# Kernel tuning notes

Measured on AMD Instinct MI355X. Metric: run time of the kernel, lower is better.

## Reference

```python
import jax, jax.numpy as jnp
import numpy as np

DIM = 768
NUM_HEADS = 12
HEAD_DIM = DIM // NUM_HEADS
HIDDEN = 4 * DIM
EPS = 1e-6


def _linear_params(key, fan_in, fan_out):
    kw, kb = jax.random.split(key)
    bound = 1.0 / np.sqrt(fan_in)
    W = jax.random.uniform(kw, (fan_in, fan_out), jnp.float32, -bound, bound)
    b = jax.random.uniform(kb, (fan_out,), jnp.float32, -bound, bound)
    return W, b


def setup_inputs() -> dict:
    key = jax.random.key(0)
    ks = jax.random.split(key, 8)
    x = jax.random.normal(ks[0], (64, 197, DIM), jnp.float32)
    Wq, bq = _linear_params(ks[1], DIM, DIM)
    Wk, bk = _linear_params(ks[2], DIM, DIM)
    Wv, bv = _linear_params(ks[3], DIM, DIM)
    Wo, bo = _linear_params(ks[4], DIM, DIM)
    W1, b1 = _linear_params(ks[5], DIM, HIDDEN)
    W2, b2 = _linear_params(ks[6], HIDDEN, DIM)
    g1 = jnp.ones((DIM,), jnp.float32); be1 = jnp.zeros((DIM,), jnp.float32)
    g2 = jnp.ones((DIM,), jnp.float32); be2 = jnp.zeros((DIM,), jnp.float32)
    return {"x": x, "Wq": Wq, "bq": bq, "Wk": Wk, "bk": bk, "Wv": Wv, "bv": bv,
            "Wo": Wo, "bo": bo, "W1": W1, "b1": b1, "W2": W2, "b2": b2,
            "g1": g1, "be1": be1, "g2": g2, "be2": be2}


def _layernorm(x, g, b):
    mu = jnp.mean(x, axis=-1, keepdims=True)
    var = jnp.mean(jnp.square(x - mu), axis=-1, keepdims=True)
    return (x - mu) * jax.lax.rsqrt(var + EPS) * g + b


def reference(x, Wq, bq, Wk, bk, Wv, bv, Wo, bo, W1, b1, W2, b2, g1, be1, g2, be2):
    B, S, D = x.shape
    # --- attention (dropout = identity at inference) ---
    q = (x @ Wq + bq).reshape(B, S, NUM_HEADS, HEAD_DIM)
    k = (x @ Wk + bk).reshape(B, S, NUM_HEADS, HEAD_DIM)
    v = (x @ Wv + bv).reshape(B, S, NUM_HEADS, HEAD_DIM)
    scale = 1.0 / np.sqrt(HEAD_DIM).astype(np.float32)
    scores = jnp.einsum('bshd,bthd->bhst', q, k) * scale  # [B,H,S,S]
    attn = jax.nn.softmax(scores, axis=-1)
    ctx = jnp.einsum('bhst,bthd->bshd', attn, v).reshape(B, S, D)
    attn_out = ctx @ Wo + bo
    x = x + _layernorm(attn_out, g1, be1)
    # --- MLP (exact GELU, dropout = identity) ---
    h = jax.nn.gelu(x @ W1 + b1, approximate=False)
    mlp_out = h @ W2 + b2
    x = x + _layernorm(mlp_out, g2, be2)
    return x
```

## Files before the change

### kernel.cpp

```cpp
#include <hip/hip_runtime.h>
#include <hip/hip_bf16.h>
#include <math.h>

#define TOK   12608
#define DMODEL 768
#define QKVN  2304
#define HID   3072
#define NH    12
#define SEQ   197
#define SPAD  256
#define SROW  208
#define NBH   768

typedef __attribute__((ext_vector_type(8))) __bf16 bf16x8;
typedef __attribute__((ext_vector_type(4))) float  f32x4;

__device__ __forceinline__ unsigned short f2b(float f){
  unsigned u = __builtin_bit_cast(unsigned, f);
  u += 0x7FFFu + ((u >> 16) & 1u);
  return (unsigned short)(u >> 16);
}
__device__ __forceinline__ float b2f(unsigned short h){
  unsigned u = ((unsigned)h) << 16;
  return __builtin_bit_cast(float, u);
}

#define GLD16(g, l) __builtin_amdgcn_global_load_lds( \
    (const __attribute__((address_space(1))) void*)(g), \
    (__attribute__((address_space(3))) void*)(l), 16, 0, 0)

__global__ void cvt_x(const float* __restrict__ x, unsigned short* __restrict__ xb, int n){
  int idx = (blockIdx.x * blockDim.x + threadIdx.x) * 4;
  if (idx < n){
    float4 v = *reinterpret_cast<const float4*>(x + idx);
    ushort4 o; o.x = f2b(v.x); o.y = f2b(v.y); o.z = f2b(v.z); o.w = f2b(v.w);
    *reinterpret_cast<ushort4*>(xb + idx) = o;
  }
}

__global__ void wt_t(const float* __restrict__ W, unsigned short* __restrict__ Wt, int K, int N){
  __shared__ float tile[32][33];
  int k0 = blockIdx.y * 32, n0 = blockIdx.x * 32;
  int tx = threadIdx.x & 31, ty = threadIdx.x >> 5;
#pragma unroll
  for (int i = 0; i < 32; i += 8)
    tile[ty + i][tx] = W[(size_t)(k0 + ty + i) * N + n0 + tx];
  __syncthreads();
#pragma unroll
  for (int i = 0; i < 32; i += 8)
    Wt[(size_t)(n0 + ty + i) * K + k0 + tx] = f2b(tile[tx][ty + i]);
}

__global__ void cat_bias(const float* __restrict__ a, const float* __restrict__ b,
                         const float* __restrict__ c, float* __restrict__ o){
  int i = blockIdx.x * blockDim.x + threadIdx.x;
  if (i < 768) o[i] = a[i];
  else if (i < 1536) o[i] = b[i - 768];
  else if (i < 2304) o[i] = c[i - 1536];
}

template<int ACT>
__global__ __launch_bounds__(256)
void gemm_nt(const unsigned short* __restrict__ A,
             const unsigned short* __restrict__ Bt,
             const float* __restrict__ bias,
             unsigned short* __restrict__ C,
             int M, int N, int K)
{
  __shared__ unsigned short As[128 * 32];
  __shared__ unsigned short Bs[128 * 32];
  const int nb = N >> 7;
  const int bm = blockIdx.x / nb;
  const int bn = blockIdx.x - bm * nb;
  const int m0 = bm << 7, n0 = bn << 7;
  const int tid = threadIdx.x;
  const int lane = tid & 63;
  const int wid = tid >> 6;

  const int r  = tid >> 2;
  const int kk = (tid & 3) << 3;
  const unsigned short* gA1 = A  + (size_t)min(m0 + r,      M - 1) * K + kk;
  const unsigned short* gA2 = A  + (size_t)min(m0 + r + 64, M - 1) * K + kk;
  const unsigned short* gB1 = Bt + (size_t)(n0 + r)      * K + kk;
  const unsigned short* gB2 = Bt + (size_t)(n0 + r + 64) * K + kk;

  char* ldsA = (char*)As + wid * 1024;
  char* ldsB = (char*)Bs + wid * 1024;

  const int fr = lane & 15;
  const int kg = (lane >> 4) << 3;
  const int wm = (wid >> 1) << 6;
  const int wn = (wid & 1) << 6;

  f32x4 acc[4][4] = {};

  for (int kt = 0; kt < K; kt += 32){
    __syncthreads();
    GLD16(gA1 + kt, ldsA);
    GLD16(gA2 + kt, ldsA + 4096);
    GLD16(gB1 + kt, ldsB);
    GLD16(gB2 + kt, ldsB + 4096);
    __syncthreads();

    bf16x8 af[4], bfv[4];
#pragma unroll
    for (int i = 0; i < 4; i++)
      af[i]  = *reinterpret_cast<const bf16x8*>(&As[(wm + i * 16 + fr) * 32 + kg]);
#pragma unroll
    for (int i = 0; i < 4; i++)
      bfv[i] = *reinterpret_cast<const bf16x8*>(&Bs[(wn + i * 16 + fr) * 32 + kg]);
#pragma unroll
    for (int mi = 0; mi < 4; mi++)
#pragma unroll
      for (int ni = 0; ni < 4; ni++)
        acc[mi][ni] = __builtin_amdgcn_mfma_f32_16x16x32_bf16(af[mi], bfv[ni], acc[mi][ni], 0, 0, 0);
  }

  const int rbase = m0 + wm + ((lane >> 4) << 2);
#pragma unroll
  for (int ni = 0; ni < 4; ni++){
    const int cc = n0 + wn + ni * 16 + fr;
    const float bv = bias[cc];
#pragma unroll
    for (int mi = 0; mi < 4; mi++){
      const int rr0 = rbase + mi * 16;
#pragma unroll
      for (int j = 0; j < 4; j++){
        int rr = rr0 + j;
        if (rr < M){
          float v = acc[mi][ni][j] + bv;
          if (ACT == 1) v = 0.5f * v * (1.0f + erff(v * 0.70710678118f));
          C[(size_t)rr * N + cc] = f2b(v);
        }
      }
    }
  }
}

__global__ __launch_bounds__(256)
void attn_scores(const unsigned short* __restrict__ qkv, unsigned short* __restrict__ P)
{
  const int gid = blockIdx.x;
  const int nt = gid & 1;
  const int mt = (gid >> 1) % 7;
  const int bh = gid / 14;
  const int b = bh / NH, h = bh - b * NH;
  const int lane = threadIdx.x & 63, wid = threadIdx.x >> 6;
  const int m0 = mt * 32 + (wid >> 1) * 16;
  const int n0 = nt * 128 + (wid & 1) * 64;
  const size_t qbase = (size_t)b * SEQ * QKVN + h * 64;
  const size_t kbase = qbase + 768;
  const int fr = lane & 15;
  const int kg = (lane >> 4) << 3;
  const int ar = min(m0 + fr, SEQ - 1);

  f32x4 acc[4] = {};
#pragma unroll
  for (int ks = 0; ks < 64; ks += 32){
    bf16x8 af = *reinterpret_cast<const bf16x8*>(&qkv[qbase + (size_t)ar * QKVN + ks + kg]);
#pragma unroll
    for (int ni = 0; ni < 4; ni++){
      int t = min(n0 + ni * 16 + fr, SEQ - 1);
      bf16x8 bv = *reinterpret_cast<const bf16x8*>(&qkv[kbase + (size_t)t * QKVN + ks + kg]);
      acc[ni] = __builtin_amdgcn_mfma_f32_16x16x32_bf16(af, bv, acc[ni], 0, 0, 0);
    }
  }
  const int rbase = m0 + ((lane >> 4) << 2);
#pragma unroll
  for (int ni = 0; ni < 4; ni++){
    int cc = n0 + ni * 16 + fr;
#pragma unroll
    for (int j = 0; j < 4; j++){
      int rr = rbase + j;
      if (rr < SEQ)
        P[((size_t)bh * SROW + rr) * SPAD + cc] = f2b(acc[ni][j] * 0.125f);
    }
  }
}

__global__ __launch_bounds__(256)
void softmax_k(unsigned short* __restrict__ P)
{
  const int idx = blockIdx.x * 4 + (threadIdx.x >> 6);
  const int bh = idx / SEQ;
  const int s  = idx - bh * SEQ;
  unsigned short* p = P + ((size_t)bh * SROW + s) * SPAD;
  const int lane = threadIdx.x & 63;
  float v[4];
  ushort4 u = *reinterpret_cast<const ushort4*>(p + lane * 4);
  v[0] = b2f(u.x); v[1] = b2f(u.y); v[2] = b2f(u.z); v[3] = b2f(u.w);
  float m = -1e30f;
#pragma unroll
  for (int j = 0; j < 4; j++){
    if (lane * 4 + j < SEQ) m = fmaxf(m, v[j]); else v[j] = -1e30f;
  }
#pragma unroll
  for (int o = 32; o > 0; o >>= 1) m = fmaxf(m, __shfl_xor(m, o));
  float sum = 0.f;
#pragma unroll
  for (int j = 0; j < 4; j++){ v[j] = __expf(v[j] - m); sum += v[j]; }
#pragma unroll
  for (int o = 32; o > 0; o >>= 1) sum += __shfl_xor(sum, o);
  const float inv = 1.0f / sum;
  ushort4 o4;
  o4.x = f2b(v[0] * inv); o4.y = f2b(v[1] * inv);
  o4.z = f2b(v[2] * inv); o4.w = f2b(v[3] * inv);
  *reinterpret_cast<ushort4*>(p + lane * 4) = o4;
}

__global__ __launch_bounds__(256)
void vtrans(const unsigned short* __restrict__ qkv, unsigned short* __restrict__ VT)
{
  const int bh = blockIdx.x;
  const int b = bh / NH, h = bh - b * NH;
  __shared__ unsigned short t[SROW][66];
  const size_t vbase = (size_t)b * SEQ * QKVN + 1536 + h * 64;
  const int lane = threadIdx.x & 63, wid = threadIdx.x >> 6;
  for (int s = wid; s < SROW; s += 4){
    unsigned short val = 0;
    if (s < SEQ) val = qkv[vbase + (size_t)s * QKVN + lane];
    t[s][lane] = val;
  }
  __syncthreads();
  unsigned short* o = VT + (size_t)bh * 64 * SPAD;
  const int tid = threadIdx.x;
#pragma unroll
  for (int i = 0; i < 64; i++){
    int idx = tid + i * 256;
    int d = idx >> 8, tt = idx & 255;
    o[idx] = (tt < SROW) ? t[tt][d] : (unsigned short)0;
  }
}

__global__ __launch_bounds__(256)
void attn_ctx(const unsigned short* __restrict__ P,
              const unsigned short* __restrict__ VT,
              unsigned short* __restrict__ ctx)
{
  const int mt = blockIdx.x & 3;
  const int bh = blockIdx.x >> 2;
  const int b = bh / NH, h = bh - b * NH;
  const int lane = threadIdx.x & 63, wid = threadIdx.x >> 6;
  const int m0 = mt * 64 + wid * 16;
  const unsigned short* Pr = P  + (size_t)bh * SROW * SPAD;
  const unsigned short* Vr = VT + (size_t)bh * 64 * SPAD;
  const int fr = lane & 15;
  const int kg = (lane >> 4) << 3;
  const int ar = min(m0 + fr, SEQ - 1);

  f32x4 acc[4] = {};
#pragma unroll
  for (int ks = 0; ks < SPAD; ks += 32){
    bf16x8 af = *reinterpret_cast<const bf16x8*>(&Pr[(size_t)ar * SPAD + ks + kg]);
#pragma unroll
    for (int ni = 0; ni < 4; ni++){
      bf16x8 bv = *reinterpret_cast<const bf16x8*>(&Vr[(size_t)(ni * 16 + fr) * SPAD + ks + kg]);
      acc[ni] = __builtin_amdgcn_mfma_f32_16x16x32_bf16(af, bv, acc[ni], 0, 0, 0);
    }
  }
  const int rbase = m0 + ((lane >> 4) << 2);
#pragma unroll
  for (int ni = 0; ni < 4; ni++){
    int d = ni * 16 + fr;
#pragma unroll
    for (int j = 0; j < 4; j++){
      int rr = rbase + j;
      if (rr < SEQ)
        ctx[((size_t)b * SEQ + rr) * DMODEL + h * 64 + d] = f2b(acc[ni][j]);
    }
  }
}

template<int RESF32, int OUTF32>
__global__ __launch_bounds__(256)
void ln_res(const unsigned short* __restrict__ y,
            const void* __restrict__ res,
            const float* __restrict__ g,
            const float* __restrict__ be,
            void* __restrict__ out)
{
  const int row = blockIdx.x * 4 + (threadIdx.x >> 6);
  const int lane = threadIdx.x & 63;
  const int c0 = lane * 12;
  const unsigned short* yr = y + (size_t)row * DMODEL + c0;
  float v[12];
#pragma unroll
  for (int i = 0; i < 3; i++){
    ushort4 u = *reinterpret_cast<const ushort4*>(yr + i * 4);
    v[i*4+0] = b2f(u.x); v[i*4+1] = b2f(u.y); v[i*4+2] = b2f(u.z); v[i*4+3] = b2f(u.w);
  }
  float s = 0.f;
#pragma unroll
  for (int i = 0; i < 12; i++) s += v[i];
#pragma unroll
  for (int o = 32; o > 0; o >>= 1) s += __shfl_xor(s, o);
  const float mu = s * (1.0f / 768.0f);
  float vs = 0.f;
#pragma unroll
  for (int i = 0; i < 12; i++){ float d = v[i] - mu; vs += d * d; }
#pragma unroll
  for (int o = 32; o > 0; o >>= 1) vs += __shfl_xor(vs, o);
  const float rstd = rsqrtf(vs * (1.0f / 768.0f) + 1e-6f);
  float ov[12];
#pragma unroll
  for (int i = 0; i < 12; i++){
    float rv;
    if (RESF32) rv = ((const float*)res)[(size_t)row * DMODEL + c0 + i];
    else        rv = b2f(((const unsigned short*)res)[(size_t)row * DMODEL + c0 + i]);
    ov[i] = (v[i] - mu) * rstd * g[c0 + i] + be[c0 + i] + rv;
  }
  if (OUTF32){
    float* o = (float*)out + (size_t)row * DMODEL + c0;
#pragma unroll
    for (int i = 0; i < 3; i++)
      *reinterpret_cast<float4*>(o + i * 4) = *reinterpret_cast<float4*>(&ov[i * 4]);
  } else {
    unsigned short* o = (unsigned short*)out + (size_t)row * DMODEL + c0;
    unsigned short ob[12];
#pragma unroll
    for (int i = 0; i < 12; i++) ob[i] = f2b(ov[i]);
#pragma unroll
    for (int i = 0; i < 3; i++)
      *reinterpret_cast<ushort4*>(o + i * 4) = *reinterpret_cast<ushort4*>(&ob[i * 4]);
  }
}

extern "C" void kernel_launch(void* const* d_in, const int* in_sizes, int n_in,
                              void* d_out, int out_size, void* d_ws, size_t ws_size,
                              hipStream_t stream)
{
  const float* x   = (const float*)d_in[0];
  const float* Wq  = (const float*)d_in[1];
  const float* bq  = (const float*)d_in[2];
  const float* Wk  = (const float*)d_in[3];
  const float* bk  = (const float*)d_in[4];
  const float* Wv  = (const float*)d_in[5];
  const float* bv  = (const float*)d_in[6];
  const float* Wo  = (const float*)d_in[7];
  const float* bo  = (const float*)d_in[8];
  const float* W1  = (const float*)d_in[9];
  const float* b1  = (const float*)d_in[10];
  const float* W2  = (const float*)d_in[11];
  const float* b2  = (const float*)d_in[12];
  const float* g1  = (const float*)d_in[13];
  const float* be1 = (const float*)d_in[14];
  const float* g2  = (const float*)d_in[15];
  const float* be2 = (const float*)d_in[16];

  char* w = (char*)d_ws;
  size_t off = 0;
  auto alloc = [&](size_t bytes){ void* p = w + off; off = (off + bytes + 255) & ~(size_t)255; return p; };
  unsigned short* wqkvt = (unsigned short*)alloc((size_t)QKVN * DMODEL * 2);
  unsigned short* wot   = (unsigned short*)alloc((size_t)DMODEL * DMODEL * 2);
  unsigned short* w1t   = (unsigned short*)alloc((size_t)HID * DMODEL * 2);
  unsigned short* w2t   = (unsigned short*)alloc((size_t)DMODEL * HID * 2);
  float*          bqkv  = (float*)alloc((size_t)QKVN * 4);
  unsigned short* xb    = (unsigned short*)alloc((size_t)TOK * DMODEL * 2);
  unsigned short* qkvb  = (unsigned short*)alloc((size_t)TOK * QKVN * 2);
  unsigned short* vtb   = (unsigned short*)alloc((size_t)NBH * 64 * SPAD * 2);
  unsigned short* Pb    = (unsigned short*)alloc((size_t)NBH * SROW * SPAD * 2);
  unsigned short* aob   = (unsigned short*)alloc((size_t)TOK * DMODEL * 2);
  unsigned short* x1b   = (unsigned short*)alloc((size_t)TOK * DMODEL * 2);
  unsigned short* ctxb  = xb;
  unsigned short* hb    = Pb;
  unsigned short* mob   = vtb;

  const int mtiles = (TOK + 127) / 128;

  cvt_x<<<(TOK * DMODEL / 4 + 255) / 256, 256, 0, stream>>>(x, xb, TOK * DMODEL);
  wt_t<<<dim3(DMODEL/32, DMODEL/32), 256, 0, stream>>>(Wq, wqkvt, DMODEL, DMODEL);
  wt_t<<<dim3(DMODEL/32, DMODEL/32), 256, 0, stream>>>(Wk, wqkvt + (size_t)DMODEL*DMODEL, DMODEL, DMODEL);
  wt_t<<<dim3(DMODEL/32, DMODEL/32), 256, 0, stream>>>(Wv, wqkvt + (size_t)2*DMODEL*DMODEL, DMODEL, DMODEL);
  wt_t<<<dim3(DMODEL/32, DMODEL/32), 256, 0, stream>>>(Wo, wot, DMODEL, DMODEL);
  wt_t<<<dim3(HID/32, DMODEL/32), 256, 0, stream>>>(W1, w1t, DMODEL, HID);
  wt_t<<<dim3(DMODEL/32, HID/32), 256, 0, stream>>>(W2, w2t, HID, DMODEL);
  cat_bias<<<9, 256, 0, stream>>>(bq, bk, bv, bqkv);

  gemm_nt<0><<<mtiles * (QKVN/128), 256, 0, stream>>>(xb, wqkvt, bqkv, qkvb, TOK, QKVN, DMODEL);
  attn_scores<<<NBH * 14, 256, 0, stream>>>(qkvb, Pb);
  softmax_k<<<NBH * SEQ / 4, 256, 0, stream>>>(Pb);
  vtrans<<<NBH, 256, 0, stream>>>(qkvb, vtb);
  attn_ctx<<<NBH * 4, 256, 0, stream>>>(Pb, vtb, ctxb);
  gemm_nt<0><<<mtiles * (DMODEL/128), 256, 0, stream>>>(ctxb, wot, bo, aob, TOK, DMODEL, DMODEL);
  ln_res<1,0><<<TOK / 4, 256, 0, stream>>>(aob, x, g1, be1, x1b);
  gemm_nt<1><<<mtiles * (HID/128), 256, 0, stream>>>(x1b, w1t, b1, hb, TOK, HID, DMODEL);
  gemm_nt<0><<<mtiles * (DMODEL/128), 256, 0, stream>>>(hb, w2t, b2, mob, TOK, DMODEL, HID);
  ln_res<0,1><<<TOK / 4, 256, 0, stream>>>(mob, x1b, g2, be2, d_out);
}
```

Before: 751.1 us.

## Double-buffer LDS tiles in the bf16 GEMM to overlap loads with MFMA

The GEMM kernel now keeps two LDS buffers for the A and B tiles. It issues the global-to-LDS loads for the next K slice before running the MFMAs on the current slice, and uses a single barrier per iteration instead of two. The aim is to hide global load latency behind matrix math and cut barrier stalls. In exchange, shared memory per block doubles, which may lower occupancy.

```diff
diff --git a/kernel.cpp b/kernel.cpp
--- a/kernel.cpp
+++ b/kernel.cpp
@@ -67,8 +67,8 @@
              unsigned short* __restrict__ C,
              int M, int N, int K)
 {
-  __shared__ unsigned short As[128 * 32];
-  __shared__ unsigned short Bs[128 * 32];
+  __shared__ unsigned short As[2][128 * 32];
+  __shared__ unsigned short Bs[2][128 * 32];
   const int nb = N >> 7;
   const int bm = blockIdx.x / nb;
   const int bn = blockIdx.x - bm * nb;
@@ -84,9 +84,6 @@
   const unsigned short* gB1 = Bt + (size_t)(n0 + r)      * K + kk;
   const unsigned short* gB2 = Bt + (size_t)(n0 + r + 64) * K + kk;
 
-  char* ldsA = (char*)As + wid * 1024;
-  char* ldsB = (char*)Bs + wid * 1024;
-
   const int fr = lane & 15;
   const int kg = (lane >> 4) << 3;
   const int wm = (wid >> 1) << 6;
@@ -94,26 +91,45 @@
 
   f32x4 acc[4][4] = {};
 
-  for (int kt = 0; kt < K; kt += 32){
-    __syncthreads();
-    GLD16(gA1 + kt, ldsA);
-    GLD16(gA2 + kt, ldsA + 4096);
-    GLD16(gB1 + kt, ldsB);
-    GLD16(gB2 + kt, ldsB + 4096);
-    __syncthreads();
+  const int nk = K >> 5;
+
+  {
+    char* ldsA = (char*)As[0] + wid * 1024;
+    char* ldsB = (char*)Bs[0] + wid * 1024;
+    GLD16(gA1, ldsA);
+    GLD16(gA2, ldsA + 4096);
+    GLD16(gB1, ldsB);
+    GLD16(gB2, ldsB + 4096);
+  }
+  __syncthreads();
+
+  int cur = 0;
+  for (int it = 0; it < nk; ++it){
+    if (it + 1 < nk){
+      const int ktn = (it + 1) << 5;
+      char* ldsA = (char*)As[cur ^ 1] + wid * 1024;
+      char* ldsB = (char*)Bs[cur ^ 1] + wid * 1024;
+      GLD16(gA1 + ktn, ldsA);
+      GLD16(gA2 + ktn, ldsA + 4096);
+      GLD16(gB1 + ktn, ldsB);
+      GLD16(gB2 + ktn, ldsB + 4096);
+    }
 
     bf16x8 af[4], bfv[4];
 #pragma unroll
     for (int i = 0; i < 4; i++)
-      af[i]  = *reinterpret_cast<const bf16x8*>(&As[(wm + i * 16 + fr) * 32 + kg]);
+      af[i]  = *reinterpret_cast<const bf16x8*>(&As[cur][(wm + i * 16 + fr) * 32 + kg]);
 #pragma unroll
     for (int i = 0; i < 4; i++)
-      bfv[i] = *reinterpret_cast<const bf16x8*>(&Bs[(wn + i * 16 + fr) * 32 + kg]);
+      bfv[i] = *reinterpret_cast<const bf16x8*>(&Bs[cur][(wn + i * 16 + fr) * 32 + kg]);
 #pragma unroll
     for (int mi = 0; mi < 4; mi++)
 #pragma unroll
       for (int ni = 0; ni < 4; ni++)
         acc[mi][ni] = __builtin_amdgcn_mfma_f32_16x16x32_bf16(af[mi], bfv[ni], acc[mi][ni], 0, 0, 0);
+
+    __syncthreads();
+    cur ^= 1;
   }
 
   const int rbase = m0 + wm + ((lane >> 4) << 2);
```

Result: faster. 727.5 us (-3.1%).

## Triple-buffer GEMM LDS tiles with async global-to-LDS prefetch two stages ahead

Applied to the files above, without the earlier changes.

The bf16 MFMA GEMM now keeps three LDS buffers for A and B and issues the direct global-to-LDS loads for tile it+2 while computing tile it. Explicit vmcnt waits and a single barrier per iteration replace the two __syncthreads around each load. The goal is to hide global load latency behind MFMA work. In exchange, LDS use triples (48KB per block), which may lower occupancy, and correctness now depends on the manual vmcnt counting.

```diff
diff --git a/kernel.cpp b/kernel.cpp
--- a/kernel.cpp
+++ b/kernel.cpp
@@ -67,8 +67,8 @@
              unsigned short* __restrict__ C,
              int M, int N, int K)
 {
-  __shared__ unsigned short As[128 * 32];
-  __shared__ unsigned short Bs[128 * 32];
+  __shared__ unsigned short As[3][128 * 32];
+  __shared__ unsigned short Bs[3][128 * 32];
   const int nb = N >> 7;
   const int bm = blockIdx.x / nb;
   const int bn = blockIdx.x - bm * nb;
@@ -84,36 +84,51 @@
   const unsigned short* gB1 = Bt + (size_t)(n0 + r)      * K + kk;
   const unsigned short* gB2 = Bt + (size_t)(n0 + r + 64) * K + kk;
 
-  char* ldsA = (char*)As + wid * 1024;
-  char* ldsB = (char*)Bs + wid * 1024;
-
   const int fr = lane & 15;
   const int kg = (lane >> 4) << 3;
   const int wm = (wid >> 1) << 6;
   const int wn = (wid & 1) << 6;
 
   f32x4 acc[4][4] = {};
-
-  for (int kt = 0; kt < K; kt += 32){
-    __syncthreads();
+  const int nk = K >> 5;
+
+  auto stage = [&](int t, int b){
+    const int kt = t << 5;
+    char* ldsA = (char*)As[b] + wid * 1024;
+    char* ldsB = (char*)Bs[b] + wid * 1024;
     GLD16(gA1 + kt, ldsA);
     GLD16(gA2 + kt, ldsA + 4096);
     GLD16(gB1 + kt, ldsB);
     GLD16(gB2 + kt, ldsB + 4096);
-    __syncthreads();
+  };
+
+  stage(0, 0);
+  stage(1, 1);
+  asm volatile("s_waitcnt vmcnt(4)" ::: "memory");
+  __builtin_amdgcn_s_barrier();
+  asm volatile("" ::: "memory");
+
+  for (int it = 0; it < nk; ++it){
+    const int cur = it % 3;
+    if (it + 2 < nk) stage(it + 2, (it + 2) % 3);
 
     bf16x8 af[4], bfv[4];
 #pragma unroll
     for (int i = 0; i < 4; i++)
-      af[i]  = *reinterpret_cast<const bf16x8*>(&As[(wm + i * 16 + fr) * 32 + kg]);
+      af[i]  = *reinterpret_cast<const bf16x8*>(&As[cur][(wm + i * 16 + fr) * 32 + kg]);
 #pragma unroll
     for (int i = 0; i < 4; i++)
-      bfv[i] = *reinterpret_cast<const bf16x8*>(&Bs[(wn + i * 16 + fr) * 32 + kg]);
+      bfv[i] = *reinterpret_cast<const bf16x8*>(&Bs[cur][(wn + i * 16 + fr) * 32 + kg]);
 #pragma unroll
     for (int mi = 0; mi < 4; mi++)
 #pragma unroll
       for (int ni = 0; ni < 4; ni++)
         acc[mi][ni] = __builtin_amdgcn_mfma_f32_16x16x32_bf16(af[mi], bfv[ni], acc[mi][ni], 0, 0, 0);
+
+    if (it + 2 < nk) asm volatile("s_waitcnt vmcnt(4)" ::: "memory");
+    else             asm volatile("s_waitcnt vmcnt(0)" ::: "memory");
+    __builtin_amdgcn_s_barrier();
+    asm volatile("" ::: "memory");
   }
 
   const int rbase = m0 + wm + ((lane >> 4) << 2);
```

Measured after the change: 735.0 us. 1.02x faster.
